# Kernel tuning notes

Measured on AMD Instinct MI355X. Metric: run time of the kernel, lower is better.

The kernel has to match this reference:

```python
import jax, jax.numpy as jnp
import numpy as np

N, DEG, IN_DIM, HID, OUT = 50000, 32, 256, 256, 128

def setup_inputs() -> dict:
    key = jax.random.key(0)
    k1, k2, k3, k4, k5, k6 = jax.random.split(key, 6)
    node_features = jax.random.normal(k1, (N, IN_DIM), dtype=jnp.float32)
    neighbor_idx = jax.random.randint(k2, (N, DEG), 0, N)
    scale1 = 1.0 / np.sqrt(2 * IN_DIM)
    scale2 = 1.0 / np.sqrt(HID)
    W1 = jax.random.normal(k3, (HID, 2 * IN_DIM), dtype=jnp.float32) * scale1
    b1 = jax.random.normal(k4, (HID,), dtype=jnp.float32) * scale1
    W2 = jax.random.normal(k5, (OUT, HID), dtype=jnp.float32) * scale2
    b2 = jax.random.normal(k6, (OUT,), dtype=jnp.float32) * scale2
    return {"node_features": node_features, "neighbor_idx": neighbor_idx,
            "W1": W1, "b1": b1, "W2": W2, "b2": b2}

def reference(node_features, neighbor_idx, W1, b1, W2, b2):
    # Layer 0 (mean aggregator, with neighbors):
    # gather [N, DEG, IN_DIM] neighbor features, mean over DEG
    nbr_mean = jnp.mean(node_features[neighbor_idx], axis=1)  # [N, IN_DIM]
    combined = jnp.concatenate([node_features, nbr_mean], axis=-1)  # [N, 2*IN_DIM]
    h = jax.nn.relu(combined @ W1.T + b1)  # [N, HID]
    # Layer 1: empty neighbor list -> linear_without_neighbors + relu
    out = jax.nn.relu(h @ W2.T + b2)  # [N, OUT]
    return out
```

## Files before the change

### kernel.cpp

```cpp
#include <hip/hip_runtime.h>
#include <stdint.h>

#define N_NODES 50000
#define DEG     32
#define IN_DIM  256
#define K1      512
#define HID     256
#define OUT_DIM 128

#define NCHUNK  4
#define CDIM    64
#define SLICE8  ((size_t)N_NODES * CDIM)
#define GT      16

#define MT     32
#define NTILES ((N_NODES + MT - 1) / MT)
#define GBLK   256
#define CSTR   520
#define HSTR   264

typedef __bf16 bf16x8 __attribute__((ext_vector_type(8)));
typedef float  f32x4  __attribute__((ext_vector_type(4)));
typedef float  f32x2  __attribute__((ext_vector_type(2)));

#define PIN(x) asm volatile("" : "+v"(x))

__device__ __forceinline__ unsigned short f2bf(float f) {
    union { float f; unsigned u; } v; v.f = f;
    unsigned r = v.u + 0x7fffu + ((v.u >> 16) & 1u);
    return (unsigned short)(r >> 16);
}
__device__ __forceinline__ int clampN(int v) {
    return v < 0 ? 0 : (v >= N_NODES ? N_NODES - 1 : v);
}
__device__ __forceinline__ void async_copy16(const void* g, void* l) {
    __builtin_amdgcn_global_load_lds(
        (const __attribute__((address_space(1))) void*)g,
        (__attribute__((address_space(3))) void*)l, 16, 0, 0);
}

#define FEAT_BLKS ((N_NODES + 7) / 8)
__global__ __launch_bounds__(256)
void prep_all(const float* __restrict__ feat,
              const float* __restrict__ W1, const float* __restrict__ W2,
              const int*   __restrict__ nbr,
              unsigned short* __restrict__ featb,
              unsigned char*  __restrict__ featF8,
              unsigned short* __restrict__ W1b, unsigned short* __restrict__ W2b,
              unsigned short* __restrict__ nbr16)
{
    const int t = threadIdx.x;
    if (blockIdx.x < FEAT_BLKS) {
        const int node = blockIdx.x * 8 + (t >> 5);
        const int seg  = t & 31;
        if (node < N_NODES) {
            const float4* src = (const float4*)(feat + (size_t)node * IN_DIM + seg * 8);
            float4 f0 = src[0], f1 = src[1];
            ushort4 o0, o1;
            o0.x = f2bf(f0.x); o0.y = f2bf(f0.y); o0.z = f2bf(f0.z); o0.w = f2bf(f0.w);
            o1.x = f2bf(f1.x); o1.y = f2bf(f1.y); o1.z = f2bf(f1.z); o1.w = f2bf(f1.w);
            unsigned short* db = featb + (size_t)node * IN_DIM + seg * 8;
            *(ushort4*)db       = o0;
            *(ushort4*)(db + 4) = o1;
            int u0 = 0, u1 = 0;
            u0 = __builtin_amdgcn_cvt_pk_fp8_f32(f0.x, f0.y, u0, false);
            u0 = __builtin_amdgcn_cvt_pk_fp8_f32(f0.z, f0.w, u0, true);
            u1 = __builtin_amdgcn_cvt_pk_fp8_f32(f1.x, f1.y, u1, false);
            u1 = __builtin_amdgcn_cvt_pk_fp8_f32(f1.z, f1.w, u1, true);
            const int c   = seg >> 3;
            const int off = (seg & 7) * 8;
            unsigned char* d8 = featF8 + (size_t)c * SLICE8 + (size_t)node * CDIM + off;
            ((int*)d8)[0] = u0;
            ((int*)d8)[1] = u1;
        }
    } else {
        const int bid = blockIdx.x - FEAT_BLKS;
        const int stride = 256 * 256 * 4;
        const int tid4 = (bid * 256 + t) * 4;
        for (int i = tid4; i < HID * K1; i += stride) {
            float4 f = *(const float4*)(W1 + i);
            ushort4 o; o.x = f2bf(f.x); o.y = f2bf(f.y); o.z = f2bf(f.z); o.w = f2bf(f.w);
            *(ushort4*)(W1b + i) = o;
        }
        for (int i = tid4; i < OUT_DIM * HID; i += stride) {
            float4 f = *(const float4*)(W2 + i);
            ushort4 o; o.x = f2bf(f.x); o.y = f2bf(f.y); o.z = f2bf(f.z); o.w = f2bf(f.w);
            *(ushort4*)(W2b + i) = o;
        }
        for (int i = tid4; i < N_NODES * DEG; i += stride) {
            int4 v = *(const int4*)(nbr + i);
            ushort4 o;
            o.x = (unsigned short)clampN(v.x); o.y = (unsigned short)clampN(v.y);
            o.z = (unsigned short)clampN(v.z); o.w = (unsigned short)clampN(v.w);
            *(ushort4*)(nbr16 + i) = o;
        }
    }
}

__global__ __launch_bounds__(256)
void gather_mean_fp8(const unsigned char*  __restrict__ featF8,
                     const unsigned short* __restrict__ nbr16,
                     unsigned short*       __restrict__ meanb)
{
    __shared__ unsigned short sIdx[GT * DEG];
    const int tid  = threadIdx.x;
    const int c    = blockIdx.y;
    const int base = blockIdx.x * GT;

    if (tid < 128) {
        *(ushort4*)(sIdx + tid * 4) =
            *(const ushort4*)(nbr16 + (size_t)base * DEG + tid * 4);
    }
    __syncthreads();

    const unsigned char* slice = featF8 + (size_t)c * SLICE8;
    const int grp = tid >> 4;
    const int ln  = tid & 15;
    const unsigned short* idxr = sIdx + grp * DEG;

    unsigned vv[DEG];
    #pragma unroll
    for (int j = 0; j < DEG; ++j) {
        int nb = idxr[j];
        vv[j] = *(const unsigned*)(slice + (size_t)nb * CDIM + ln * 4);
    }
    float s0 = 0.f, s1 = 0.f, s2 = 0.f, s3 = 0.f;
    #pragma unroll
    for (int j = 0; j < DEG; ++j) {
        f32x2 lo = __builtin_amdgcn_cvt_pk_f32_fp8(vv[j], false);
        f32x2 hi = __builtin_amdgcn_cvt_pk_f32_fp8(vv[j], true);
        s0 += lo[0]; s1 += lo[1]; s2 += hi[0]; s3 += hi[1];
    }
    const float sc = 1.0f / 32.0f;
    ushort4 o;
    o.x = f2bf(s0 * sc); o.y = f2bf(s1 * sc);
    o.z = f2bf(s2 * sc); o.w = f2bf(s3 * sc);
    const int node = base + grp;
    *(ushort4*)(meanb + (size_t)node * IN_DIM + c * CDIM + ln * 4) = o;
}

__global__ __launch_bounds__(512, 2)
void sage_gemm_dbuf(const unsigned short* __restrict__ featb,
                    const unsigned short* __restrict__ meanb,
                    const unsigned short* __restrict__ W1b,
                    const float*          __restrict__ b1,
                    const unsigned short* __restrict__ W2b,
                    const float*          __restrict__ b2,
                    float*                __restrict__ out)
{
    __shared__ __align__(16) unsigned short sC[2][MT * CSTR];
    __shared__ __align__(16) unsigned short sH[MT * HSTR];

    const int tid  = threadIdx.x;
    const int lane = tid & 63;
    const int wave = tid >> 6;
    const int r    = lane & 15;
    const int q    = lane >> 4;

    bf16x8 w1f[2][16];
    #pragma unroll
    for (int nt = 0; nt < 2; ++nt) {
        const size_t nrow = (size_t)(wave * 32 + nt * 16 + r) * K1;
        #pragma unroll
        for (int kk = 0; kk < 16; ++kk) {
            w1f[nt][kk] = *(const bf16x8*)(W1b + nrow + kk * 32 + q * 8);
            PIN(w1f[nt][kk]);
        }
    }
    bf16x8 w2f[8];
    {
        const size_t orow = (size_t)(wave * 16 + r) * HID;
        #pragma unroll
        for (int kk = 0; kk < 8; ++kk) {
            w2f[kk] = *(const bf16x8*)(W2b + orow + kk * 32 + q * 8);
            PIN(w2f[kk]);
        }
    }
    const float bias1a = b1[wave * 32 + r];
    const float bias1b = b1[wave * 32 + 16 + r];
    const float bias2  = b2[wave * 16 + r];

    auto stage = [&](int tile, int buf) {
        const int base = tile * MT;
        #pragma unroll
        for (int j = 0; j < 4; ++j) {
            const int i = wave * 4 + j;
            int node = base + i;
            if (node >= N_NODES) node = N_NODES - 1;
            const unsigned short* g = (lane < 32)
                ? featb + (size_t)node * IN_DIM + lane * 8
                : meanb + (size_t)node * IN_DIM + (lane - 32) * 8;
            async_copy16(g, &sC[buf][i * CSTR]);
        }
    };

    int tile = blockIdx.x;
    if (tile < NTILES) stage(tile, 0);
    int buf = 0;

    for (; tile < NTILES; tile += GBLK) {
        __syncthreads();

        const int nxt = tile + GBLK;
        if (nxt < NTILES) stage(nxt, buf ^ 1);

        {
            f32x4 acc[2][2];
            #pragma unroll
            for (int mt = 0; mt < 2; ++mt)
                #pragma unroll
                for (int nt = 0; nt < 2; ++nt)
                    acc[mt][nt] = (f32x4){0.f, 0.f, 0.f, 0.f};

            #pragma unroll
            for (int kk = 0; kk < 16; ++kk) {
                bf16x8 a0 = *(const bf16x8*)(&sC[buf][r * CSTR + kk * 32 + q * 8]);
                bf16x8 a1 = *(const bf16x8*)(&sC[buf][(16 + r) * CSTR + kk * 32 + q * 8]);
                acc[0][0] = __builtin_amdgcn_mfma_f32_16x16x32_bf16(a0, w1f[0][kk], acc[0][0], 0, 0, 0);
                acc[1][0] = __builtin_amdgcn_mfma_f32_16x16x32_bf16(a1, w1f[0][kk], acc[1][0], 0, 0, 0);
                acc[0][1] = __builtin_amdgcn_mfma_f32_16x16x32_bf16(a0, w1f[1][kk], acc[0][1], 0, 0, 0);
                acc[1][1] = __builtin_amdgcn_mfma_f32_16x16x32_bf16(a1, w1f[1][kk], acc[1][1], 0, 0, 0);
            }
            #pragma unroll
            for (int nt = 0; nt < 2; ++nt) {
                const int n = wave * 32 + nt * 16 + r;
                const float bias = nt ? bias1b : bias1a;
                #pragma unroll
                for (int mt = 0; mt < 2; ++mt)
                    #pragma unroll
                    for (int g = 0; g < 4; ++g) {
                        const int m = mt * 16 + q * 4 + g;
                        float v = acc[mt][nt][g] + bias;
                        sH[m * HSTR + n] = f2bf(v > 0.f ? v : 0.f);
                    }
            }
        }
        __syncthreads();

        {
            f32x4 acc3[2];
            acc3[0] = (f32x4){0.f, 0.f, 0.f, 0.f};
            acc3[1] = (f32x4){0.f, 0.f, 0.f, 0.f};
            #pragma unroll
            for (int kk = 0; kk < 8; ++kk) {
                bf16x8 h0 = *(const bf16x8*)(&sH[r * HSTR + kk * 32 + q * 8]);
                bf16x8 h1 = *(const bf16x8*)(&sH[(16 + r) * HSTR + kk * 32 + q * 8]);
                acc3[0] = __builtin_amdgcn_mfma_f32_16x16x32_bf16(h0, w2f[kk], acc3[0], 0, 0, 0);
                acc3[1] = __builtin_amdgcn_mfma_f32_16x16x32_bf16(h1, w2f[kk], acc3[1], 0, 0, 0);
            }
            const int base = tile * MT;
            const int o = wave * 16 + r;
            #pragma unroll
            for (int mt = 0; mt < 2; ++mt)
                #pragma unroll
                for (int g = 0; g < 4; ++g) {
                    const int m = mt * 16 + q * 4 + g;
                    const int node = base + m;
                    if (node < N_NODES) {
                        float v = acc3[mt][g] + bias2;
                        out[(size_t)node * OUT_DIM + o] = v > 0.f ? v : 0.f;
                    }
                }
        }
        buf ^= 1;
    }
}

__global__ __launch_bounds__(256)
void sage_naive(const float* __restrict__ feat, const int* __restrict__ nbr,
                const float* __restrict__ W1, const float* __restrict__ b1,
                const float* __restrict__ W2, const float* __restrict__ b2,
                float* __restrict__ out) {
    __shared__ float comb[K1];
    __shared__ float h[HID];
    const int node = blockIdx.x;
    const int t = threadIdx.x;
    comb[t] = feat[(size_t)node * IN_DIM + t];
    float acc = 0.f;
    for (int d = 0; d < DEG; ++d) {
        int nb = clampN(nbr[node * DEG + d]);
        acc += feat[(size_t)nb * IN_DIM + t];
    }
    comb[IN_DIM + t] = acc * (1.0f / 32.0f);
    __syncthreads();
    float s = b1[t];
    for (int k = 0; k < K1; ++k) s += comb[k] * W1[(size_t)t * K1 + k];
    h[t] = s > 0.f ? s : 0.f;
    __syncthreads();
    if (t < OUT_DIM) {
        float s2 = b2[t];
        for (int k = 0; k < HID; ++k) s2 += h[k] * W2[(size_t)t * HID + k];
        out[(size_t)node * OUT_DIM + t] = s2 > 0.f ? s2 : 0.f;
    }
}

extern "C" void kernel_launch(void* const* d_in, const int* in_sizes, int n_in,
                              void* d_out, int out_size, void* d_ws, size_t ws_size,
                              hipStream_t stream) {
    const float* feat = (const float*)d_in[0];
    const int*   nbr  = (const int*)d_in[1];
    const float* W1   = (const float*)d_in[2];
    const float* b1   = (const float*)d_in[3];
    const float* W2   = (const float*)d_in[4];
    const float* b2   = (const float*)d_in[5];
    float* out = (float*)d_out;

    const size_t feat_elems = (size_t)N_NODES * IN_DIM;
    const size_t w1_elems   = (size_t)HID * K1;
    const size_t w2_elems   = (size_t)OUT_DIM * HID;
    const size_t mean_elems = (size_t)N_NODES * IN_DIM;
    const size_t idx_elems  = (size_t)N_NODES * DEG;
    const size_t u16_elems  = feat_elems + w1_elems + w2_elems + mean_elems + idx_elems;
    const size_t need = u16_elems * sizeof(unsigned short)
                      + (size_t)NCHUNK * SLICE8;

    if (ws_size >= need) {
        unsigned short* featb  = (unsigned short*)d_ws;
        unsigned short* W1b    = featb + feat_elems;
        unsigned short* W2b    = W1b + w1_elems;
        unsigned short* meanb  = W2b + w2_elems;
        unsigned short* nbr16  = meanb + mean_elems;
        unsigned char*  featF8 = (unsigned char*)(nbr16 + idx_elems);

        prep_all<<<FEAT_BLKS + 256, 256, 0, stream>>>(feat, W1, W2, nbr,
                                                      featb, featF8, W1b, W2b, nbr16);
        gather_mean_fp8<<<dim3(N_NODES / GT, NCHUNK), 256, 0, stream>>>(featF8, nbr16, meanb);
        sage_gemm_dbuf<<<GBLK, 512, 0, stream>>>(featb, meanb, W1b, b1, W2b, b2, out);
    } else {
        sage_naive<<<N_NODES, 256, 0, stream>>>(feat, nbr, W1, b1, W2, b2, out);
    }
}
```

Before: 175.3 us.

## Fuse fp8 neighbor gather into persistent GEMM kernel with multi-stage pipeline

Removes the separate gather_mean kernel and its bf16 mean buffer round-trip through global memory. The persistent GEMM blocks now gather fp8 neighbor rows for upcoming tiles into LDS, one 64-column chunk per iteration across a four-tile lookahead, and prefetch neighbor indices five tiles ahead. The LDS layout changes to XOR-swizzled 512-byte rows without padding. This trades the extra launch and mean-buffer traffic for higher LDS use, more registers, and gather latency that now sits inside the GEMM loop with only 256 blocks.

New measurement: 189.1 us. +7.8%, slower.

```diff
diff --git a/kernel.cpp b/kernel.cpp
--- a/kernel.cpp
+++ b/kernel.cpp
@@ -11,17 +11,17 @@
 #define NCHUNK  4
 #define CDIM    64
 #define SLICE8  ((size_t)N_NODES * CDIM)
-#define GT      16
 
 #define MT     32
 #define NTILES ((N_NODES + MT - 1) / MT)
 #define GBLK   256
-#define CSTR   520
 #define HSTR   264
 
 typedef __bf16 bf16x8 __attribute__((ext_vector_type(8)));
 typedef float  f32x4  __attribute__((ext_vector_type(4)));
 typedef float  f32x2  __attribute__((ext_vector_type(2)));
+typedef unsigned short u16x8 __attribute__((ext_vector_type(8)));
+typedef unsigned int   u32x4 __attribute__((ext_vector_type(4)));
 
 #define PIN(x) asm volatile("" : "+v"(x))
 
@@ -97,59 +97,20 @@
     }
 }
 
-__global__ __launch_bounds__(256)
-void gather_mean_fp8(const unsigned char*  __restrict__ featF8,
-                     const unsigned short* __restrict__ nbr16,
-                     unsigned short*       __restrict__ meanb)
+__global__ __launch_bounds__(512, 2)
+void sage_fused(const unsigned short* __restrict__ featb,
+                const unsigned char*  __restrict__ featF8,
+                const unsigned short* __restrict__ nbr16,
+                const unsigned short* __restrict__ W1b,
+                const float*          __restrict__ b1,
+                const unsigned short* __restrict__ W2b,
+                const float*          __restrict__ b2,
+                float*                __restrict__ out)
 {
-    __shared__ unsigned short sIdx[GT * DEG];
-    const int tid  = threadIdx.x;
-    const int c    = blockIdx.y;
-    const int base = blockIdx.x * GT;
-
-    if (tid < 128) {
-        *(ushort4*)(sIdx + tid * 4) =
-            *(const ushort4*)(nbr16 + (size_t)base * DEG + tid * 4);
-    }
-    __syncthreads();
-
-    const unsigned char* slice = featF8 + (size_t)c * SLICE8;
-    const int grp = tid >> 4;
-    const int ln  = tid & 15;
-    const unsigned short* idxr = sIdx + grp * DEG;
-
-    unsigned vv[DEG];
-    #pragma unroll
-    for (int j = 0; j < DEG; ++j) {
-        int nb = idxr[j];
-        vv[j] = *(const unsigned*)(slice + (size_t)nb * CDIM + ln * 4);
-    }
-    float s0 = 0.f, s1 = 0.f, s2 = 0.f, s3 = 0.f;
-    #pragma unroll
-    for (int j = 0; j < DEG; ++j) {
-        f32x2 lo = __builtin_amdgcn_cvt_pk_f32_fp8(vv[j], false);
-        f32x2 hi = __builtin_amdgcn_cvt_pk_f32_fp8(vv[j], true);
-        s0 += lo[0]; s1 += lo[1]; s2 += hi[0]; s3 += hi[1];
-    }
-    const float sc = 1.0f / 32.0f;
-    ushort4 o;
-    o.x = f2bf(s0 * sc); o.y = f2bf(s1 * sc);
-    o.z = f2bf(s2 * sc); o.w = f2bf(s3 * sc);
-    const int node = base + grp;
-    *(ushort4*)(meanb + (size_t)node * IN_DIM + c * CDIM + ln * 4) = o;
-}
-
-__global__ __launch_bounds__(512, 2)
-void sage_gemm_dbuf(const unsigned short* __restrict__ featb,
-                    const unsigned short* __restrict__ meanb,
-                    const unsigned short* __restrict__ W1b,
-                    const float*          __restrict__ b1,
-                    const unsigned short* __restrict__ W2b,
-                    const float*          __restrict__ b2,
-                    float*                __restrict__ out)
-{
-    __shared__ __align__(16) unsigned short sC[2][MT * CSTR];
+    __shared__ __align__(16) unsigned char  sSelf[2][MT * 512];
+    __shared__ __align__(16) unsigned char  sMean[4][MT * 512];
     __shared__ __align__(16) unsigned short sH[MT * HSTR];
+    __shared__ __align__(16) unsigned short sIdx[8][MT * DEG];
 
     const int tid  = threadIdx.x;
     const int lane = tid & 63;
@@ -180,46 +141,98 @@
     const float bias1b = b1[wave * 32 + 16 + r];
     const float bias2  = b2[wave * 16 + r];
 
-    auto stage = [&](int tile, int buf) {
-        const int base = tile * MT;
-        #pragma unroll
-        for (int j = 0; j < 4; ++j) {
-            const int i = wave * 4 + j;
-            int node = base + i;
-            if (node >= N_NODES) node = N_NODES - 1;
-            const unsigned short* g = (lane < 32)
-                ? featb + (size_t)node * IN_DIM + lane * 8
-                : meanb + (size_t)node * IN_DIM + (lane - 32) * 8;
-            async_copy16(g, &sC[buf][i * CSTR]);
-        }
-    };
-
-    int tile = blockIdx.x;
-    if (tile < NTILES) stage(tile, 0);
-    int buf = 0;
-
-    for (; tile < NTILES; tile += GBLK) {
-        __syncthreads();
-
-        const int nxt = tile + GBLK;
-        if (nxt < NTILES) stage(nxt, buf ^ 1);
-
+    const int t0   = blockIdx.x;
+    const int imax = (NTILES - 1 - t0) / GBLK + 1;
+
+    const int gs = tid >> 7;
+    const int gm = (tid >> 2) & 31;
+    const int gl = tid & 3;
+
+    {
+        const int e = t0 * (MT * DEG) + tid * 2;
+        unsigned v = (e + 1 < N_NODES * DEG) ? *(const unsigned*)(nbr16 + e) : 0u;
+        *(unsigned*)(&sIdx[0][tid * 2]) = v;
+    }
+    __syncthreads();
+
+    for (int i = -4; i < imax; ++i) {
         {
-            f32x4 acc[2][2];
+            const int tn = t0 + (i + 1) * GBLK;
+            if (tn >= 0 && tn < NTILES) {
+                unsigned char* dstBase = sSelf[(i + 1) & 1];
+                #pragma unroll
+                for (int j = 0; j < 2; ++j) {
+                    const int p = wave * 2 + j;
+                    int node = tn * MT + p * 2 + (lane >> 5);
+                    if (node >= N_NODES) node = N_NODES - 1;
+                    const int g = (lane & 31) ^ (node & 7);
+                    async_copy16(featb + (size_t)node * IN_DIM + g * 8,
+                                 dstBase + p * 1024);
+                }
+            }
+        }
+        const int ti5 = t0 + (i + 5) * GBLK;
+        unsigned idxw = 0;
+        if (ti5 < NTILES) {
+            const int e = ti5 * (MT * DEG) + tid * 2;
+            idxw = (e + 1 < N_NODES * DEG) ? *(const unsigned*)(nbr16 + e) : 0u;
+        }
+        const int c  = i & 3;
+        const int js = i + 1 + gs;
+        const int tg = t0 + js * GBLK;
+        const bool doG = (tg >= 0) && (tg < NTILES);
+        u32x4 p0 = {0u, 0u, 0u, 0u}, p1 = {0u, 0u, 0u, 0u};
+        if (doG) {
+            f32x2 ga[8];
+            #pragma unroll
+            for (int k = 0; k < 8; ++k) ga[k] = (f32x2){0.f, 0.f};
+            const unsigned char*  sl = featF8 + (size_t)c * SLICE8 + gl * 16;
+            const unsigned short* ip = &sIdx[js & 7][gm * DEG];
+            #pragma unroll
+            for (int gb = 0; gb < 4; ++gb) {
+                const u16x8 id8 = *(const u16x8*)(ip + gb * 8);
+                u32x4 vv[8];
+                #pragma unroll
+                for (int j = 0; j < 8; ++j)
+                    vv[j] = *(const u32x4*)(sl + (size_t)id8[j] * CDIM);
+                #pragma unroll
+                for (int j = 0; j < 8; ++j) {
+                    #pragma unroll
+                    for (int w = 0; w < 4; ++w) {
+                        f32x2 lo = __builtin_amdgcn_cvt_pk_f32_fp8(vv[j][w], false);
+                        f32x2 hi = __builtin_amdgcn_cvt_pk_f32_fp8(vv[j][w], true);
+                        ga[w * 2]     += lo;
+                        ga[w * 2 + 1] += hi;
+                    }
+                }
+            }
+            const float sc = 1.0f / 32.0f;
+            #pragma unroll
+            for (int k = 0; k < 4; ++k) {
+                p0[k] = (unsigned)f2bf(ga[k][0] * sc)     | ((unsigned)f2bf(ga[k][1] * sc) << 16);
+                p1[k] = (unsigned)f2bf(ga[4 + k][0] * sc) | ((unsigned)f2bf(ga[4 + k][1] * sc) << 16);
+            }
+        }
+        if (i >= 0) {
+            const unsigned char* selfB = sSelf[i & 1];
+            const unsigned char* meanB = sMean[i & 3];
+            f32x4 ac1[2][2];
             #pragma unroll
             for (int mt = 0; mt < 2; ++mt)
                 #pragma unroll
                 for (int nt = 0; nt < 2; ++nt)
-                    acc[mt][nt] = (f32x4){0.f, 0.f, 0.f, 0.f};
+                    ac1[mt][nt] = (f32x4){0.f, 0.f, 0.f, 0.f};
 
             #pragma unroll
             for (int kk = 0; kk < 16; ++kk) {
-                bf16x8 a0 = *(const bf16x8*)(&sC[buf][r * CSTR + kk * 32 + q * 8]);
-                bf16x8 a1 = *(const bf16x8*)(&sC[buf][(16 + r) * CSTR + kk * 32 + q * 8]);
-                acc[0][0] = __builtin_amdgcn_mfma_f32_16x16x32_bf16(a0, w1f[0][kk], acc[0][0], 0, 0, 0);
-                acc[1][0] = __builtin_amdgcn_mfma_f32_16x16x32_bf16(a1, w1f[0][kk], acc[1][0], 0, 0, 0);
-                acc[0][1] = __builtin_amdgcn_mfma_f32_16x16x32_bf16(a0, w1f[1][kk], acc[0][1], 0, 0, 0);
-                acc[1][1] = __builtin_amdgcn_mfma_f32_16x16x32_bf16(a1, w1f[1][kk], acc[1][1], 0, 0, 0);
+                const unsigned char* src = (kk < 8) ? selfB : meanB;
+                const int go = ((4 * (kk & 7) + q) ^ (r & 7)) * 16;
+                bf16x8 a0 = *(const bf16x8*)(src + (size_t)r * 512 + go);
+                bf16x8 a1 = *(const bf16x8*)(src + (size_t)(16 + r) * 512 + go);
+                ac1[0][0] = __builtin_amdgcn_mfma_f32_16x16x32_bf16(a0, w1f[0][kk], ac1[0][0], 0, 0, 0);
+                ac1[1][0] = __builtin_amdgcn_mfma_f32_16x16x32_bf16(a1, w1f[0][kk], ac1[1][0], 0, 0, 0);
+                ac1[0][1] = __builtin_amdgcn_mfma_f32_16x16x32_bf16(a0, w1f[1][kk], ac1[0][1], 0, 0, 0);
+                ac1[1][1] = __builtin_amdgcn_mfma_f32_16x16x32_bf16(a1, w1f[1][kk], ac1[1][1], 0, 0, 0);
             }
             #pragma unroll
             for (int nt = 0; nt < 2; ++nt) {
@@ -230,25 +243,24 @@
                     #pragma unroll
                     for (int g = 0; g < 4; ++g) {
                         const int m = mt * 16 + q * 4 + g;
-                        float v = acc[mt][nt][g] + bias;
+                        float v = ac1[mt][nt][g] + bias;
                         sH[m * HSTR + n] = f2bf(v > 0.f ? v : 0.f);
                     }
             }
         }
         __syncthreads();
-
-        {
-            f32x4 acc3[2];
-            acc3[0] = (f32x4){0.f, 0.f, 0.f, 0.f};
-            acc3[1] = (f32x4){0.f, 0.f, 0.f, 0.f};
+        if (i >= 0) {
+            f32x4 ac2[2];
+            ac2[0] = (f32x4){0.f, 0.f, 0.f, 0.f};
+            ac2[1] = (f32x4){0.f, 0.f, 0.f, 0.f};
             #pragma unroll
             for (int kk = 0; kk < 8; ++kk) {
                 bf16x8 h0 = *(const bf16x8*)(&sH[r * HSTR + kk * 32 + q * 8]);
                 bf16x8 h1 = *(const bf16x8*)(&sH[(16 + r) * HSTR + kk * 32 + q * 8]);
-                acc3[0] = __builtin_amdgcn_mfma_f32_16x16x32_bf16(h0, w2f[kk], acc3[0], 0, 0, 0);
-                acc3[1] = __builtin_amdgcn_mfma_f32_16x16x32_bf16(h1, w2f[kk], acc3[1], 0, 0, 0);
-            }
-            const int base = tile * MT;
+                ac2[0] = __builtin_amdgcn_mfma_f32_16x16x32_bf16(h0, w2f[kk], ac2[0], 0, 0, 0);
+                ac2[1] = __builtin_amdgcn_mfma_f32_16x16x32_bf16(h1, w2f[kk], ac2[1], 0, 0, 0);
+            }
+            const int base = (t0 + i * GBLK) * MT;
             const int o = wave * 16 + r;
             #pragma unroll
             for (int mt = 0; mt < 2; ++mt)
@@ -257,12 +269,21 @@
                     const int m = mt * 16 + q * 4 + g;
                     const int node = base + m;
                     if (node < N_NODES) {
-                        float v = acc3[mt][g] + bias2;
+                        float v = ac2[mt][g] + bias2;
                         out[(size_t)node * OUT_DIM + o] = v > 0.f ? v : 0.f;
                     }
                 }
         }
-        buf ^= 1;
+        if (doG) {
+            unsigned char* mb = sMean[js & 3] + gm * 512;
+            const int g0 = 8 * c + 2 * gl;
+            *(u32x4*)(mb + (size_t)((g0)     ^ (gm & 7)) * 16) = p0;
+            *(u32x4*)(mb + (size_t)((g0 + 1) ^ (gm & 7)) * 16) = p1;
+        }
+        if (ti5 < NTILES) {
+            *(unsigned*)(&sIdx[(i + 5) & 7][tid * 2]) = idxw;
+        }
+        __syncthreads();
     }
 }
 
@@ -308,9 +329,8 @@
     const size_t feat_elems = (size_t)N_NODES * IN_DIM;
     const size_t w1_elems   = (size_t)HID * K1;
     const size_t w2_elems   = (size_t)OUT_DIM * HID;
-    const size_t mean_elems = (size_t)N_NODES * IN_DIM;
     const size_t idx_elems  = (size_t)N_NODES * DEG;
-    const size_t u16_elems  = feat_elems + w1_elems + w2_elems + mean_elems + idx_elems;
+    const size_t u16_elems  = feat_elems + w1_elems + w2_elems + idx_elems;
     const size_t need = u16_elems * sizeof(unsigned short)
                       + (size_t)NCHUNK * SLICE8;
 
@@ -318,14 +338,12 @@
         unsigned short* featb  = (unsigned short*)d_ws;
         unsigned short* W1b    = featb + feat_elems;
         unsigned short* W2b    = W1b + w1_elems;
-        unsigned short* meanb  = W2b + w2_elems;
-        unsigned short* nbr16  = meanb + mean_elems;
+        unsigned short* nbr16  = W2b + w2_elems;
         unsigned char*  featF8 = (unsigned char*)(nbr16 + idx_elems);
 
         prep_all<<<FEAT_BLKS + 256, 256, 0, stream>>>(feat, W1, W2, nbr,
                                                       featb, featF8, W1b, W2b, nbr16);
-        gather_mean_fp8<<<dim3(N_NODES / GT, NCHUNK), 256, 0, stream>>>(featF8, nbr16, meanb);
-        sage_gemm_dbuf<<<GBLK, 512, 0, stream>>>(featb, meanb, W1b, b1, W2b, b2, out);
+        sage_fused<<<GBLK, 512, 0, stream>>>(featb, featF8, nbr16, W1b, b1, W2b, b2, out);
     } else {
         sage_naive<<<N_NODES, 256, 0, stream>>>(feat, nbr, W1, b1, W2, b2, out);
     }
```
